# Kernel tuning notes

Measured on AMD Instinct MI355X. Metric: run time of the kernel, lower is better.

## Reference

```python
import jax, jax.numpy as jnp
import numpy as np

B, L, C, D, K = 32, 36864, 16, 512, 24


def setup_inputs() -> dict:
    key = jax.random.key(0)
    ks = jax.random.split(key, 5)
    x = jax.random.normal(ks[0], (B, L, C), jnp.float32)
    # offset-conv weights scaled small so predicted offsets are O(0.2) (kaiming-ish but tame)
    w_off = jax.random.normal(ks[1], (2 * K, C, K), jnp.float32) * 0.01
    b_off = jax.random.normal(ks[2], (2 * K,), jnp.float32) * 0.05
    w_def = jax.random.normal(ks[3], (D, C, K), jnp.float32) * (2.0 / (C * K)) ** 0.5
    b_def = jax.random.normal(ks[4], (D,), jnp.float32) * 0.05
    return {"x": x, "w_off": w_off, "b_off": b_off, "w_def": w_def, "b_def": b_def}


def reference(x, w_off, b_off, w_def, b_def):
    # x: [B, L, C] -> torch view [B, C, 1, L]; H == 1 throughout.
    Bn, Ln, Cn = x.shape
    twoK, _, Kn = w_off.shape
    Lout = Ln // Kn
    xc = jnp.transpose(x, (0, 2, 1))                 # [B, C, L]
    xk = xc.reshape(Bn, Cn, Lout, Kn)                # stride == kernel -> non-overlapping windows
    # offset conv: [B, 2K, Lout]
    off = jnp.einsum('bclk,ock->bol', xk, w_off) + b_off[None, :, None]
    off = off.reshape(Bn, Kn, 2, Lout)               # channel 2k -> dy, 2k+1 -> dx (torchvision layout)
    dy = jnp.transpose(off[:, :, 0, :], (0, 2, 1))   # [B, Lout, K]
    dx = jnp.transpose(off[:, :, 1, :], (0, 2, 1))   # [B, Lout, K]
    # sampling positions along width; base = w_out*K + k
    base = jnp.arange(Lout * Kn, dtype=x.dtype).reshape(Lout, Kn)
    px = base[None] + dx                             # [B, Lout, K]
    # height bilinear weight: with H=1, contribution at h=0 is max(0, 1-|dy|)
    wy = jnp.maximum(jnp.array(0, x.dtype), 1.0 - jnp.abs(dy))
    # width bilinear with zero padding (torchvision bilinear_interpolate semantics)
    valid = (px > -1.0) & (px < Ln)
    x0 = jnp.floor(px)
    lw = px - x0                                     # weight for right neighbor
    i0 = x0.astype(jnp.int32)
    i1 = i0 + 1
    m0 = (valid & (i0 >= 0) & (i0 < Ln)).astype(x.dtype)
    m1 = (valid & (i1 >= 0) & (i1 < Ln)).astype(x.dtype)
    i0c = jnp.broadcast_to(jnp.clip(i0, 0, Ln - 1).reshape(Bn, 1, Lout * Kn), (Bn, Cn, Lout * Kn))
    i1c = jnp.broadcast_to(jnp.clip(i1, 0, Ln - 1).reshape(Bn, 1, Lout * Kn), (Bn, Cn, Lout * Kn))
    v0 = jnp.take_along_axis(xc, i0c, axis=2).reshape(Bn, Cn, Lout, Kn)
    v1 = jnp.take_along_axis(xc, i1c, axis=2).reshape(Bn, Cn, Lout, Kn)
    val = (v0 * ((1.0 - lw) * m0)[:, None] + v1 * (lw * m1)[:, None]) * wy[:, None]  # [B,C,Lout,K]
    out = jnp.einsum('bclk,dck->bld', val, w_def) + b_def  # [B, Lout, D]
    return out
```

## Files before the change

kernel.cpp:

```cpp
#include <hip/hip_runtime.h>
#include <stdint.h>

#define BATCH 32
#define LLEN  36864
#define CCH   16
#define DOUT  512
#define KW    24
#define LOUT  1536
#define MROWS (BATCH * LOUT)
#define CK    384
#define TWOK  48

typedef float fx4 __attribute__((ext_vector_type(4)));
typedef float f32x4 __attribute__((ext_vector_type(4)));
typedef __bf16 bf16x8 __attribute__((ext_vector_type(8)));
typedef uint32_t u32x4 __attribute__((ext_vector_type(4)));

__device__ __forceinline__ void gload16(void* lds, const void* g)
{
    __builtin_amdgcn_global_load_lds(
        (const __attribute__((address_space(1))) uint32_t*)g,
        (__attribute__((address_space(3))) uint32_t*)lds, 16, 0, 0);
}

__global__ __launch_bounds__(256) void prep_kernel(
    const float* __restrict__ w_off, const float* __restrict__ w_def,
    __bf16* __restrict__ woff_b, __bf16* __restrict__ wdef_b)
{
    int idx = blockIdx.x * 256 + threadIdx.x;
    if (idx < TWOK * CK) {
        int o = idx / CK, rem = idx % CK;
        int k = rem >> 4, c = rem & 15;
        woff_b[idx] = (__bf16)w_off[o * CK + c * KW + k];
    }
    if (idx < DOUT * CK) {
        int d = idx / CK, rem = idx % CK;
        int k = rem >> 4, c = rem & 15;
        wdef_b[idx] = (__bf16)w_def[d * CK + c * KW + k];
    }
}

__global__ __launch_bounds__(256, 3) void offsets_kernel(
    const float* __restrict__ x, const __bf16* __restrict__ woff_b,
    const float* __restrict__ b_off, uint32_t* __restrict__ dxy)
{
    __shared__ __bf16 Bs[TWOK * 392];
    __shared__ float  offS[64 * 49];

    const int t = threadIdx.x;
#pragma unroll
    for (int i = 0; i < 9; ++i) {
        int ch = t + 256 * i;
        int row = ch / 48, cc = ch % 48;
        *(u32x4*)&Bs[row * 392 + cc * 8] =
            *(const u32x4*)&woff_b[row * CK + cc * 8];
    }
    __syncthreads();

    const int wave = t >> 6, lane = t & 63;
    const int quad = lane >> 4, l16 = lane & 15;
    const int m0 = blockIdx.x * 64;
    const int row = m0 + wave * 16 + l16;
    const float* xr = x + (size_t)row * CK;

    f32x4 acc[3] = {};
#pragma unroll
    for (int ks = 0; ks < 12; ++ks) {
        int k0 = ks * 32 + quad * 8;
        fx4 a0 = *(const fx4*)&xr[k0];
        fx4 a1 = *(const fx4*)&xr[k0 + 4];
        bf16x8 af;
        af[0] = (__bf16)a0.x; af[1] = (__bf16)a0.y;
        af[2] = (__bf16)a0.z; af[3] = (__bf16)a0.w;
        af[4] = (__bf16)a1.x; af[5] = (__bf16)a1.y;
        af[6] = (__bf16)a1.z; af[7] = (__bf16)a1.w;
#pragma unroll
        for (int j = 0; j < 3; ++j) {
            bf16x8 bf = *(const bf16x8*)&Bs[(j * 16 + l16) * 392 + k0];
            acc[j] = __builtin_amdgcn_mfma_f32_16x16x32_bf16(af, bf, acc[j], 0, 0, 0);
        }
    }
#pragma unroll
    for (int j = 0; j < 3; ++j)
#pragma unroll
        for (int r = 0; r < 4; ++r)
            offS[(wave * 16 + quad * 4 + r) * 49 + j * 16 + l16] = acc[j][r];
    __syncthreads();

#pragma unroll
    for (int s = 0; s < 6; ++s) {
        int id = t + 256 * s;
        int r = id / 24, k = id - r * 24;
        float dy = offS[r * 49 + 2 * k]     + b_off[2 * k];
        float dx = offS[r * 49 + 2 * k + 1] + b_off[2 * k + 1];
        union { __bf16 h[2]; uint32_t u; } p;
        p.h[0] = (__bf16)dy; p.h[1] = (__bf16)dx;
        dxy[(size_t)m0 * KW + id] = p.u;
    }
}

#define BM 128
#define BN 512
#define BK 64

__global__ __launch_bounds__(512, 2) void gemm_fused(
    const float* __restrict__ x, const uint32_t* __restrict__ dxy,
    const __bf16* __restrict__ Bw, const float* __restrict__ bias,
    float* __restrict__ out)
{
    __shared__ __bf16 As[BM * BK];
    __shared__ __bf16 Bs[BN * BK];

    const int t = threadIdx.x;
    const int m0 = blockIdx.x * BM;
    const int wave = t >> 6, lane = t & 63;
    const int quad = lane >> 4, l16 = lane & 15;
    const int wr = wave >> 2, wc = wave & 3;

    const int mloc = t >> 2, k4 = t & 3;
    const int Mrow = m0 + mloc;
    const int b    = Mrow / LOUT;
    const int lb   = Mrow - b * LOUT;
    const float* xb = x + (size_t)b * LLEN * CCH;

    f32x4 acc[4][8] = {};

    fx4 g0[4], g1[4];
    float w0, w1;

    auto load_pair = [&](int kk) {
        union { uint32_t u; __bf16 h[2]; } p;
        p.u = dxy[(size_t)Mrow * KW + kk];
        float dy = (float)p.h[0], dx = (float)p.h[1];
        float wy  = fmaxf(0.f, 1.f - fabsf(dy));
        float px  = (float)(lb * KW + kk) + dx;
        float x0f = floorf(px);
        float lw  = px - x0f;
        int   i0  = (int)x0f;
        bool valid = (px > -1.0f) && (px < (float)LLEN);
        w0 = (valid && i0 >= 0)         ? (1.f - lw) * wy : 0.f;
        w1 = (valid && (i0 + 1) < LLEN) ? lw * wy         : 0.f;
        int i0c = min(max(i0, 0), LLEN - 1);
        int i1c = min(max(i0 + 1, 0), LLEN - 1);
        const fx4* p0 = (const fx4*)&xb[(size_t)i0c * CCH];
        const fx4* p1 = (const fx4*)&xb[(size_t)i1c * CCH];
#pragma unroll
        for (int q = 0; q < 4; ++q) { g0[q] = p0[q]; g1[q] = p1[q]; }
    };

    load_pair(k4);

    for (int kt = 0; kt < CK; kt += BK) {
        __syncthreads();
        bf16x8 oa, ob;
#pragma unroll
        for (int q = 0; q < 2; ++q) {
            fx4 v0 = g0[q], v1 = g1[q];
            oa[q * 4 + 0] = (__bf16)(w0 * v0.x + w1 * v1.x);
            oa[q * 4 + 1] = (__bf16)(w0 * v0.y + w1 * v1.y);
            oa[q * 4 + 2] = (__bf16)(w0 * v0.z + w1 * v1.z);
            oa[q * 4 + 3] = (__bf16)(w0 * v0.w + w1 * v1.w);
        }
#pragma unroll
        for (int q = 0; q < 2; ++q) {
            fx4 v0 = g0[q + 2], v1 = g1[q + 2];
            ob[q * 4 + 0] = (__bf16)(w0 * v0.x + w1 * v1.x);
            ob[q * 4 + 1] = (__bf16)(w0 * v0.y + w1 * v1.y);
            ob[q * 4 + 2] = (__bf16)(w0 * v0.z + w1 * v1.z);
            ob[q * 4 + 3] = (__bf16)(w0 * v0.w + w1 * v1.w);
        }
        int g = 2 * k4;
        *(bf16x8*)&As[mloc * BK + ((g ^ (mloc & 7)) * 8)]       = oa;
        *(bf16x8*)&As[mloc * BK + (((g + 1) ^ (mloc & 7)) * 8)] = ob;
#pragma unroll
        for (int it = 0; it < 8; ++it) {
            int q = it * 512 + t;
            int r = q >> 3, c8 = q & 7;
            int sc = c8 ^ (r & 7);
            gload16(&Bs[q * 8], Bw + (size_t)r * CK + kt + sc * 8);
        }
        __syncthreads();
        if (kt + BK < CK) load_pair((kt >> 4) + 4 + k4);
#pragma unroll
        for (int ks = 0; ks < 2; ++ks) {
            bf16x8 af[4], bfr[8];
#pragma unroll
            for (int i = 0; i < 4; ++i) {
                int row = wr * 64 + i * 16 + l16;
                af[i] = *(const bf16x8*)&As[row * BK + (((ks * 4 + quad) ^ (row & 7)) * 8)];
            }
#pragma unroll
            for (int j = 0; j < 8; ++j) {
                int col = wc * 128 + j * 16 + l16;
                bfr[j] = *(const bf16x8*)&Bs[col * BK + (((ks * 4 + quad) ^ (col & 7)) * 8)];
            }
#pragma unroll
            for (int i = 0; i < 4; ++i)
#pragma unroll
                for (int j = 0; j < 8; ++j)
                    acc[i][j] = __builtin_amdgcn_mfma_f32_16x16x32_bf16(
                        af[i], bfr[j], acc[i][j], 0, 0, 0);
        }
    }

#pragma unroll
    for (int j = 0; j < 8; ++j) {
        int col = wc * 128 + j * 16 + l16;
        float bj = bias[col];
#pragma unroll
        for (int i = 0; i < 4; ++i) {
            int rowb = m0 + wr * 64 + i * 16 + quad * 4;
#pragma unroll
            for (int r = 0; r < 4; ++r)
                out[(size_t)(rowb + r) * DOUT + col] = acc[i][j][r] + bj;
        }
    }
}

extern "C" void kernel_launch(void* const* d_in, const int* in_sizes, int n_in,
                              void* d_out, int out_size, void* d_ws, size_t ws_size,
                              hipStream_t stream)
{
    const float* x     = (const float*)d_in[0];
    const float* w_off = (const float*)d_in[1];
    const float* b_off = (const float*)d_in[2];
    const float* w_def = (const float*)d_in[3];
    const float* b_def = (const float*)d_in[4];
    float* out = (float*)d_out;

    char* ws = (char*)d_ws;
    uint32_t* dxy    = (uint32_t*)ws;
    __bf16*   wdef_b = (__bf16*)(ws + 4718592);
    __bf16*   woff_b = (__bf16*)(ws + 5111808);

    prep_kernel<<<768, 256, 0, stream>>>(w_off, w_def, woff_b, wdef_b);
    offsets_kernel<<<MROWS / 64, 256, 0, stream>>>(x, woff_b, b_off, dxy);
    gemm_fused<<<MROWS / BM, 512, 0, stream>>>(x, dxy, wdef_b, b_def, out);
}
```

Before: 206.7 us.

## Fuse offset-conv GEMM into main deformable GEMM, shrink M tile to 96

Removes the separate offsets kernel and its global dxy round trip: each GEMM block first computes the offset conv for its 96 rows using MFMA with w_off staged in LDS that is later reused for the B tile, then keeps the packed offsets in registers. The M tile shrinks from 128 to 96 so one block's rows stay inside a single batch and the accumulator footprint drops; only 384 of the 512 threads build the A tile. This saves a launch and a global write and read of the offsets, but adds a serial offset phase at the start of every block, leaves some threads idle during gather, and drops the occupancy hint from launch_bounds.

```diff
diff --git a/kernel.cpp b/kernel.cpp
--- a/kernel.cpp
+++ b/kernel.cpp
@@ -40,76 +40,20 @@
     }
 }
 
-__global__ __launch_bounds__(256, 3) void offsets_kernel(
-    const float* __restrict__ x, const __bf16* __restrict__ woff_b,
-    const float* __restrict__ b_off, uint32_t* __restrict__ dxy)
-{
-    __shared__ __bf16 Bs[TWOK * 392];
-    __shared__ float  offS[64 * 49];
-
-    const int t = threadIdx.x;
-#pragma unroll
-    for (int i = 0; i < 9; ++i) {
-        int ch = t + 256 * i;
-        int row = ch / 48, cc = ch % 48;
-        *(u32x4*)&Bs[row * 392 + cc * 8] =
-            *(const u32x4*)&woff_b[row * CK + cc * 8];
-    }
-    __syncthreads();
-
-    const int wave = t >> 6, lane = t & 63;
-    const int quad = lane >> 4, l16 = lane & 15;
-    const int m0 = blockIdx.x * 64;
-    const int row = m0 + wave * 16 + l16;
-    const float* xr = x + (size_t)row * CK;
-
-    f32x4 acc[3] = {};
-#pragma unroll
-    for (int ks = 0; ks < 12; ++ks) {
-        int k0 = ks * 32 + quad * 8;
-        fx4 a0 = *(const fx4*)&xr[k0];
-        fx4 a1 = *(const fx4*)&xr[k0 + 4];
-        bf16x8 af;
-        af[0] = (__bf16)a0.x; af[1] = (__bf16)a0.y;
-        af[2] = (__bf16)a0.z; af[3] = (__bf16)a0.w;
-        af[4] = (__bf16)a1.x; af[5] = (__bf16)a1.y;
-        af[6] = (__bf16)a1.z; af[7] = (__bf16)a1.w;
-#pragma unroll
-        for (int j = 0; j < 3; ++j) {
-            bf16x8 bf = *(const bf16x8*)&Bs[(j * 16 + l16) * 392 + k0];
-            acc[j] = __builtin_amdgcn_mfma_f32_16x16x32_bf16(af, bf, acc[j], 0, 0, 0);
-        }
-    }
-#pragma unroll
-    for (int j = 0; j < 3; ++j)
-#pragma unroll
-        for (int r = 0; r < 4; ++r)
-            offS[(wave * 16 + quad * 4 + r) * 49 + j * 16 + l16] = acc[j][r];
-    __syncthreads();
-
-#pragma unroll
-    for (int s = 0; s < 6; ++s) {
-        int id = t + 256 * s;
-        int r = id / 24, k = id - r * 24;
-        float dy = offS[r * 49 + 2 * k]     + b_off[2 * k];
-        float dx = offS[r * 49 + 2 * k + 1] + b_off[2 * k + 1];
-        union { __bf16 h[2]; uint32_t u; } p;
-        p.h[0] = (__bf16)dy; p.h[1] = (__bf16)dx;
-        dxy[(size_t)m0 * KW + id] = p.u;
-    }
-}
-
-#define BM 128
+#define BM 96
 #define BN 512
 #define BK 64
 
-__global__ __launch_bounds__(512, 2) void gemm_fused(
-    const float* __restrict__ x, const uint32_t* __restrict__ dxy,
-    const __bf16* __restrict__ Bw, const float* __restrict__ bias,
-    float* __restrict__ out)
+__global__ __launch_bounds__(512) void gemm_fused(
+    const float* __restrict__ x, const __bf16* __restrict__ woff_b,
+    const float* __restrict__ b_off, const __bf16* __restrict__ Bw,
+    const float* __restrict__ bias, float* __restrict__ out)
 {
     __shared__ __bf16 As[BM * BK];
-    __shared__ __bf16 Bs[BN * BK];
+    __shared__ char  smemB[BN * BK * 2];
+    __bf16* Bs    = (__bf16*)smemB;
+    __bf16* WoffS = (__bf16*)smemB;
+    float*  offS  = (float*)(smemB + 38144);
 
     const int t = threadIdx.x;
     const int m0 = blockIdx.x * BM;
@@ -119,18 +63,70 @@
 
     const int mloc = t >> 2, k4 = t & 3;
     const int Mrow = m0 + mloc;
-    const int b    = Mrow / LOUT;
+    const int b    = m0 / LOUT;
     const int lb   = Mrow - b * LOUT;
     const float* xb = x + (size_t)b * LLEN * CCH;
 
-    f32x4 acc[4][8] = {};
-
+#pragma unroll
+    for (int i = 0; i < 5; ++i) {
+        int q = t + 512 * i;
+        if (q < 2304) {
+            int row = q / 48, cc = q - row * 48;
+            *(u32x4*)&WoffS[row * 392 + cc * 8] =
+                *(const u32x4*)&woff_b[row * CK + cc * 8];
+        }
+    }
+    __syncthreads();
+
+    if (wave < 6) {
+        const float* xr = x + (size_t)(m0 + wave * 16 + l16) * CK;
+        f32x4 oacc[3] = {};
+#pragma unroll
+        for (int ks = 0; ks < 12; ++ks) {
+            int k0 = ks * 32 + quad * 8;
+            fx4 a0 = *(const fx4*)&xr[k0];
+            fx4 a1 = *(const fx4*)&xr[k0 + 4];
+            bf16x8 af;
+            af[0] = (__bf16)a0.x; af[1] = (__bf16)a0.y;
+            af[2] = (__bf16)a0.z; af[3] = (__bf16)a0.w;
+            af[4] = (__bf16)a1.x; af[5] = (__bf16)a1.y;
+            af[6] = (__bf16)a1.z; af[7] = (__bf16)a1.w;
+#pragma unroll
+            for (int j = 0; j < 3; ++j) {
+                bf16x8 bf = *(const bf16x8*)&WoffS[(j * 16 + l16) * 392 + k0];
+                oacc[j] = __builtin_amdgcn_mfma_f32_16x16x32_bf16(af, bf, oacc[j], 0, 0, 0);
+            }
+        }
+        float bo[3];
+#pragma unroll
+        for (int j = 0; j < 3; ++j) bo[j] = b_off[j * 16 + l16];
+#pragma unroll
+        for (int j = 0; j < 3; ++j)
+#pragma unroll
+            for (int r = 0; r < 4; ++r)
+                offS[(wave * 16 + quad * 4 + r) * 49 + j * 16 + l16] = oacc[j][r] + bo[j];
+    }
+    __syncthreads();
+
+    uint32_t dxyr[6];
+    if (t < 4 * BM) {
+#pragma unroll
+        for (int cc = 0; cc < 6; ++cc) {
+            int kk = 4 * cc + k4;
+            float dy = offS[mloc * 49 + 2 * kk];
+            float dx = offS[mloc * 49 + 2 * kk + 1];
+            union { __bf16 h[2]; uint32_t u; } p;
+            p.h[0] = (__bf16)dy; p.h[1] = (__bf16)dx;
+            dxyr[cc] = p.u;
+        }
+    }
+
+    f32x4 acc[3][8] = {};
     fx4 g0[4], g1[4];
     float w0, w1;
 
-    auto load_pair = [&](int kk) {
-        union { uint32_t u; __bf16 h[2]; } p;
-        p.u = dxy[(size_t)Mrow * KW + kk];
+    auto load_pair = [&](uint32_t pk, int kk) {
+        union { uint32_t u; __bf16 h[2]; } p; p.u = pk;
         float dy = (float)p.h[0], dx = (float)p.h[1];
         float wy  = fmaxf(0.f, 1.f - fabsf(dy));
         float px  = (float)(lb * KW + kk) + dx;
@@ -148,30 +144,34 @@
         for (int q = 0; q < 4; ++q) { g0[q] = p0[q]; g1[q] = p1[q]; }
     };
 
-    load_pair(k4);
-
-    for (int kt = 0; kt < CK; kt += BK) {
+    if (t < 4 * BM) load_pair(dxyr[0], k4);
+
+#pragma unroll
+    for (int cc = 0; cc < 6; ++cc) {
+        const int kt = cc * BK;
         __syncthreads();
-        bf16x8 oa, ob;
-#pragma unroll
-        for (int q = 0; q < 2; ++q) {
-            fx4 v0 = g0[q], v1 = g1[q];
-            oa[q * 4 + 0] = (__bf16)(w0 * v0.x + w1 * v1.x);
-            oa[q * 4 + 1] = (__bf16)(w0 * v0.y + w1 * v1.y);
-            oa[q * 4 + 2] = (__bf16)(w0 * v0.z + w1 * v1.z);
-            oa[q * 4 + 3] = (__bf16)(w0 * v0.w + w1 * v1.w);
-        }
-#pragma unroll
-        for (int q = 0; q < 2; ++q) {
-            fx4 v0 = g0[q + 2], v1 = g1[q + 2];
-            ob[q * 4 + 0] = (__bf16)(w0 * v0.x + w1 * v1.x);
-            ob[q * 4 + 1] = (__bf16)(w0 * v0.y + w1 * v1.y);
-            ob[q * 4 + 2] = (__bf16)(w0 * v0.z + w1 * v1.z);
-            ob[q * 4 + 3] = (__bf16)(w0 * v0.w + w1 * v1.w);
-        }
-        int g = 2 * k4;
-        *(bf16x8*)&As[mloc * BK + ((g ^ (mloc & 7)) * 8)]       = oa;
-        *(bf16x8*)&As[mloc * BK + (((g + 1) ^ (mloc & 7)) * 8)] = ob;
+        if (t < 4 * BM) {
+            bf16x8 oa, ob;
+#pragma unroll
+            for (int q = 0; q < 2; ++q) {
+                fx4 v0 = g0[q], v1 = g1[q];
+                oa[q * 4 + 0] = (__bf16)(w0 * v0.x + w1 * v1.x);
+                oa[q * 4 + 1] = (__bf16)(w0 * v0.y + w1 * v1.y);
+                oa[q * 4 + 2] = (__bf16)(w0 * v0.z + w1 * v1.z);
+                oa[q * 4 + 3] = (__bf16)(w0 * v0.w + w1 * v1.w);
+            }
+#pragma unroll
+            for (int q = 0; q < 2; ++q) {
+                fx4 v0 = g0[q + 2], v1 = g1[q + 2];
+                ob[q * 4 + 0] = (__bf16)(w0 * v0.x + w1 * v1.x);
+                ob[q * 4 + 1] = (__bf16)(w0 * v0.y + w1 * v1.y);
+                ob[q * 4 + 2] = (__bf16)(w0 * v0.z + w1 * v1.z);
+                ob[q * 4 + 3] = (__bf16)(w0 * v0.w + w1 * v1.w);
+            }
+            int g = 2 * k4;
+            *(bf16x8*)&As[mloc * BK + ((g ^ (mloc & 7)) * 8)]       = oa;
+            *(bf16x8*)&As[mloc * BK + (((g + 1) ^ (mloc & 7)) * 8)] = ob;
+        }
 #pragma unroll
         for (int it = 0; it < 8; ++it) {
             int q = it * 512 + t;
@@ -180,13 +180,14 @@
             gload16(&Bs[q * 8], Bw + (size_t)r * CK + kt + sc * 8);
         }
         __syncthreads();
-        if (kt + BK < CK) load_pair((kt >> 4) + 4 + k4);
+        if (cc + 1 < 6 && t < 4 * BM)
+            load_pair(dxyr[cc + 1], 4 * (cc + 1) + k4);
 #pragma unroll
         for (int ks = 0; ks < 2; ++ks) {
-            bf16x8 af[4], bfr[8];
-#pragma unroll
-            for (int i = 0; i < 4; ++i) {
-                int row = wr * 64 + i * 16 + l16;
+            bf16x8 af[3], bfr[8];
+#pragma unroll
+            for (int i = 0; i < 3; ++i) {
+                int row = wr * 48 + i * 16 + l16;
                 af[i] = *(const bf16x8*)&As[row * BK + (((ks * 4 + quad) ^ (row & 7)) * 8)];
             }
 #pragma unroll
@@ -195,7 +196,7 @@
                 bfr[j] = *(const bf16x8*)&Bs[col * BK + (((ks * 4 + quad) ^ (col & 7)) * 8)];
             }
 #pragma unroll
-            for (int i = 0; i < 4; ++i)
+            for (int i = 0; i < 3; ++i)
 #pragma unroll
                 for (int j = 0; j < 8; ++j)
                     acc[i][j] = __builtin_amdgcn_mfma_f32_16x16x32_bf16(
@@ -208,8 +209,8 @@
         int col = wc * 128 + j * 16 + l16;
         float bj = bias[col];
 #pragma unroll
-        for (int i = 0; i < 4; ++i) {
-            int rowb = m0 + wr * 64 + i * 16 + quad * 4;
+        for (int i = 0; i < 3; ++i) {
+            int rowb = m0 + wr * 48 + i * 16 + quad * 4;
 #pragma unroll
             for (int r = 0; r < 4; ++r)
                 out[(size_t)(rowb + r) * DOUT + col] = acc[i][j][r] + bj;
@@ -229,11 +230,9 @@
     float* out = (float*)d_out;
 
     char* ws = (char*)d_ws;
-    uint32_t* dxy    = (uint32_t*)ws;
-    __bf16*   wdef_b = (__bf16*)(ws + 4718592);
-    __bf16*   woff_b = (__bf16*)(ws + 5111808);
+    __bf16* wdef_b = (__bf16*)ws;
+    __bf16* woff_b = (__bf16*)(ws + 393216);
 
     prep_kernel<<<768, 256, 0, stream>>>(w_off, w_def, woff_b, wdef_b);
-    offsets_kernel<<<MROWS / 64, 256, 0, stream>>>(x, woff_b, b_off, dxy);
-    gemm_fused<<<MROWS / BM, 512, 0, stream>>>(x, dxy, wdef_b, b_def, out);
-}
+    gemm_fused<<<MROWS / BM, 512, 0, stream>>>(x, woff_b, b_off, wdef_b, b_def, out);
+}
```

New measurement: 196.6 us. 4.9% less time.
